# Performance work log

Measured on AMD Instinct MI355X. Metric: run time of the kernel, lower is better.

The kernel has to match this reference:

```python
import jax, jax.numpy as jnp
import numpy as np

EPS = 1e-6
B, H, S, D = 8, 16, 4096, 64


def setup_inputs() -> dict:
    key = jax.random.key(0)
    k1, k2, k3 = jax.random.split(key, 3)
    return {
        "keys": jax.random.normal(k1, (B, H, S, D), dtype=jnp.float32),
        "values": jax.random.normal(k2, (B, H, S, D), dtype=jnp.float32),
        "queries": jax.random.normal(k3, (B, H, S, D), dtype=jnp.float32),
    }


def reference(keys, values, queries):
    # update: accumulate outer-product associative memory per (batch, head)
    # M[b,h] = sum_s k_s outer v_s  -> [B, H, D, D]
    M = jnp.einsum("bhsd,bhse->bhde", keys, values)
    # normalizer z[b,h] = sum_s k_s -> [B, H, D]
    z = jnp.sum(keys, axis=2)
    # retrieve: out = (q @ M) / (q . z + eps)
    num = jnp.einsum("bhqd,bhde->bhqe", queries, M)        # [B, H, S, D]
    den = jnp.einsum("bhqd,bhd->bhq", queries, z) + EPS     # [B, H, S]
    return num / den[..., None]
```

## Files before the change

### kernel.cpp

```cpp
#include <hip/hip_runtime.h>

constexpr int Bc = 8, Hc = 16, Sc = 4096, Dc = 64;
constexpr int BH = Bc * Hc;
constexpr int STG = 16;
constexpr int MM = Dc * Dc;
constexpr int QT = 128;

template<int SSL>
__global__ __launch_bounds__(256, 4) void k1_accum(const float* __restrict__ K,
                                                   const float* __restrict__ V,
                                                   float* __restrict__ Pm,
                                                   double* __restrict__ Pz) {
  constexpr int CH = Sc / SSL;
  constexpr int NS = CH / STG;
  const int blk = blockIdx.x;
  const int bh = blk / SSL;
  const int ck = blk % SSL;
  const size_t base = ((size_t)bh * Sc + (size_t)ck * CH) * Dc;
  const float4* gk4 = (const float4*)(K + base);
  const float4* gv4 = (const float4*)(V + base);

  __shared__ __align__(16) float smem[4096];

  const int tid = threadIdx.x;
  const int w = tid >> 6;
  const int l = tid & 63;
  const int d0 = (l >> 3) * 8;
  const int e0 = (l & 7) * 8;

  float acc[8][8] = {};
  double zacc = 0.0;

  const int srow = tid >> 4;
  const int scol = (tid & 15) * 4;

  float4 rk = gk4[tid], rv = gv4[tid];
  *(float4*)&smem[srow * 64 + scol] = rk;
  *(float4*)&smem[2048 + srow * 64 + scol] = rv;
  __syncthreads();

  for (int st = 0; st < NS; ++st) {
    const int cur = st & 1, nxt = cur ^ 1;
    if (st + 1 < NS) {
      rk = gk4[(st + 1) * 256 + tid];
      rv = gv4[(st + 1) * 256 + tid];
    }
    const float* lkc = &smem[cur * 1024];
    const float* lvc = &smem[2048 + cur * 1024];
    #pragma unroll
    for (int r = 0; r < 4; ++r) {
      const int row = w * 4 + r;
      const float4 ka = *(const float4*)&lkc[row * 64 + d0];
      const float4 kb = *(const float4*)&lkc[row * 64 + d0 + 4];
      const float4 va = *(const float4*)&lvc[row * 64 + e0];
      const float4 vb = *(const float4*)&lvc[row * 64 + e0 + 4];
      const float kk[8] = {ka.x, ka.y, ka.z, ka.w, kb.x, kb.y, kb.z, kb.w};
      const float vv[8] = {va.x, va.y, va.z, va.w, vb.x, vb.y, vb.z, vb.w};
      #pragma unroll
      for (int a = 0; a < 8; ++a)
        #pragma unroll
        for (int b = 0; b < 8; ++b)
          acc[a][b] = fmaf(kk[a], vv[b], acc[a][b]);
    }
    #pragma unroll
    for (int r = 0; r < 4; ++r)
      zacc += (double)lkc[(w * 4 + r) * 64 + l];
    if (st + 1 < NS) {
      *(float4*)&smem[nxt * 1024 + srow * 64 + scol] = rk;
      *(float4*)&smem[2048 + nxt * 1024 + srow * 64 + scol] = rv;
    }
    __syncthreads();
  }

  #pragma unroll
  for (int p = 0; p < 4; ++p) {
    if (w == p) {
      #pragma unroll
      for (int a = 0; a < 8; ++a) {
        float* dst = &smem[(d0 + a) * 64 + e0];
        float4 lo = make_float4(acc[a][0], acc[a][1], acc[a][2], acc[a][3]);
        float4 hi = make_float4(acc[a][4], acc[a][5], acc[a][6], acc[a][7]);
        if (p == 0) {
          *(float4*)dst = lo; *(float4*)(dst + 4) = hi;
        } else {
          float4 olo = *(float4*)dst, ohi = *(float4*)(dst + 4);
          olo.x += lo.x; olo.y += lo.y; olo.z += lo.z; olo.w += lo.w;
          ohi.x += hi.x; ohi.y += hi.y; ohi.z += hi.z; ohi.w += hi.w;
          *(float4*)dst = olo; *(float4*)(dst + 4) = ohi;
        }
      }
    }
    __syncthreads();
  }

  float* pd = Pm + ((size_t)ck * BH + bh) * MM;
  #pragma unroll
  for (int j = 0; j < 4; ++j) {
    const int idx = tid + j * 256;
    ((float4*)pd)[idx] = *(const float4*)&smem[idx * 4];
  }
  Pz[((size_t)(ck * 4 + w) * BH + bh) * Dc + l] = zacc;
}

__global__ __launch_bounds__(256) void k2_reduce(const float* __restrict__ Pm,
                                                 const double* __restrict__ Pz,
                                                 float* __restrict__ Fm,
                                                 float* __restrict__ Fz,
                                                 int ss) {
  const int i = blockIdx.x * 256 + threadIdx.x;
  const int nm = BH * MM;
  if (i < nm) {
    float s = 0.f;
    for (int c = 0; c < ss; ++c) s += Pm[(size_t)c * nm + i];
    Fm[i] = s;
  }
  const int nz = BH * Dc;
  if (i < nz) {
    double s = 0.0;
    const int np = ss * 4;
    for (int c = 0; c < np; ++c) s += Pz[(size_t)c * nz + i];
    Fz[i] = (float)s;
  }
}

__global__ __launch_bounds__(256) void k3_retrieve(const float* __restrict__ Q,
                                                   const float* __restrict__ Fm,
                                                   const float* __restrict__ Fz,
                                                   float* __restrict__ O) {
  const int blk = blockIdx.x;
  const int bh = blk >> 5;
  const int row0 = (blk & 31) * QT;

  __shared__ __align__(16) float lm[Dc][Dc];
  __shared__ __align__(16) float lq[QT][68];
  __shared__ __align__(16) float lz[Dc];

  const int tid = threadIdx.x;

  const float4* gm4 = (const float4*)(Fm + (size_t)bh * MM);
  float4* lm4 = (float4*)&lm[0][0];
  #pragma unroll
  for (int j = 0; j < 4; ++j) lm4[tid + j * 256] = gm4[tid + j * 256];
  if (tid < Dc) lz[tid] = Fz[(size_t)bh * Dc + tid];

  const float4* gq4 = (const float4*)(Q + ((size_t)bh * Sc + row0) * Dc);
  #pragma unroll
  for (int j = 0; j < 8; ++j) {
    const int i4 = tid + j * 256;
    const float4 v = gq4[i4];
    const int f = i4 * 4;
    *(float4*)&lq[f >> 6][f & 63] = v;
  }
  __syncthreads();

  const int rg = tid >> 3;
  const int cg = tid & 7;
  const int r0 = rg * 4;
  const int e0 = cg * 8;

  float acc[4][8] = {};
  double den[4] = {0.0, 0.0, 0.0, 0.0};

  #pragma unroll
  for (int ds = 0; ds < 16; ++ds) {
    const int d0 = ds * 4;
    const float4 z4 = *(const float4*)&lz[d0];
    const float* zf = (const float*)&z4;
    float4 q4[4];
    #pragma unroll
    for (int r = 0; r < 4; ++r) q4[r] = *(const float4*)&lq[r0 + r][d0];
    const float* qf[4] = {(const float*)&q4[0], (const float*)&q4[1],
                          (const float*)&q4[2], (const float*)&q4[3]};
    #pragma unroll
    for (int i = 0; i < 4; ++i) {
      const float4 ma = *(const float4*)&lm[d0 + i][e0];
      const float4 mb = *(const float4*)&lm[d0 + i][e0 + 4];
      const float mf[8] = {ma.x, ma.y, ma.z, ma.w, mb.x, mb.y, mb.z, mb.w};
      const double zd = (double)zf[i];
      #pragma unroll
      for (int r = 0; r < 4; ++r) {
        const float qs = qf[r][i];
        den[r] += (double)qs * zd;
        #pragma unroll
        for (int j = 0; j < 8; ++j)
          acc[r][j] = fmaf(qs, mf[j], acc[r][j]);
      }
    }
  }

  #pragma unroll
  for (int r = 0; r < 4; ++r) {
    const double iv = 1.0 / (den[r] + 1e-6);
    float* go = O + ((size_t)bh * Sc + row0 + r0 + r) * Dc + e0;
    ((float4*)go)[0] = make_float4((float)((double)acc[r][0] * iv),
                                   (float)((double)acc[r][1] * iv),
                                   (float)((double)acc[r][2] * iv),
                                   (float)((double)acc[r][3] * iv));
    ((float4*)go)[1] = make_float4((float)((double)acc[r][4] * iv),
                                   (float)((double)acc[r][5] * iv),
                                   (float)((double)acc[r][6] * iv),
                                   (float)((double)acc[r][7] * iv));
  }
}

extern "C" void kernel_launch(void* const* d_in, const int* in_sizes, int n_in,
                              void* d_out, int out_size, void* d_ws, size_t ws_size,
                              hipStream_t stream) {
  const float* K = (const float*)d_in[0];
  const float* V = (const float*)d_in[1];
  const float* Q = (const float*)d_in[2];
  float* O = (float*)d_out;

  const size_t need16 = (size_t)16 * BH * MM * 4 + (size_t)BH * MM * 4 +
                        (size_t)16 * 4 * BH * Dc * 8 + (size_t)BH * Dc * 4;
  const int ss = (ws_size >= need16) ? 16 : 8;

  float* Pm = (float*)d_ws;
  float* Fm = Pm + (size_t)ss * BH * MM;
  double* Pz = (double*)(Fm + (size_t)BH * MM);
  float* Fz = (float*)(Pz + (size_t)ss * 4 * BH * Dc);

  if (ss == 16)
    hipLaunchKernelGGL(k1_accum<16>, dim3(BH * 16), dim3(256), 0, stream, K, V, Pm, Pz);
  else
    hipLaunchKernelGGL(k1_accum<8>, dim3(BH * 8), dim3(256), 0, stream, K, V, Pm, Pz);
  hipLaunchKernelGGL(k2_reduce, dim3((BH * MM + 255) / 256), dim3(256), 0, stream, Pm, Pz, Fm, Fz, ss);
  hipLaunchKernelGGL(k3_retrieve, dim3(BH * (Sc / QT)), dim3(256), 0, stream, Q, Fm, Fz, O);
}
```

Baseline: 192.5 us.

## Load K/V rows directly per wave with register double-buffering, drop LDS staging

The accumulation kernel no longer stages K/V tiles through shared memory with block-wide barriers. Each wave now streams its own contiguous range of rows straight from global memory into registers, using a two-deep software pipeline of loads. The split count is fixed at 8 chunks instead of choosing 16 from workspace size, and the reduction loops are unrolled with compile-time trip counts. This removes LDS traffic and per-stage syncs, but each lane issues many redundant global loads (64 lanes read the same row), depends on cache for reuse, and has half the blocks to hide latency.

```diff
diff --git a/kernel.cpp b/kernel.cpp
--- a/kernel.cpp
+++ b/kernel.cpp
@@ -2,76 +2,71 @@
 
 constexpr int Bc = 8, Hc = 16, Sc = 4096, Dc = 64;
 constexpr int BH = Bc * Hc;
-constexpr int STG = 16;
+constexpr int SS = 8;
+constexpr int CHUNK = Sc / SS;
+constexpr int WROWS = CHUNK / 4;
 constexpr int MM = Dc * Dc;
+constexpr int NZP = SS * 4;
 constexpr int QT = 128;
 
-template<int SSL>
-__global__ __launch_bounds__(256, 4) void k1_accum(const float* __restrict__ K,
-                                                   const float* __restrict__ V,
-                                                   float* __restrict__ Pm,
-                                                   double* __restrict__ Pz) {
-  constexpr int CH = Sc / SSL;
-  constexpr int NS = CH / STG;
+__global__ __launch_bounds__(256) void k1_accum(const float* __restrict__ K,
+                                                const float* __restrict__ V,
+                                                float* __restrict__ Pm,
+                                                double* __restrict__ Pz) {
   const int blk = blockIdx.x;
-  const int bh = blk / SSL;
-  const int ck = blk % SSL;
-  const size_t base = ((size_t)bh * Sc + (size_t)ck * CH) * Dc;
-  const float4* gk4 = (const float4*)(K + base);
-  const float4* gv4 = (const float4*)(V + base);
-
-  __shared__ __align__(16) float smem[4096];
-
+  const int bh = blk >> 3;
+  const int ck = blk & 7;
   const int tid = threadIdx.x;
   const int w = tid >> 6;
   const int l = tid & 63;
   const int d0 = (l >> 3) * 8;
   const int e0 = (l & 7) * 8;
 
+  const size_t rbase = ((size_t)bh * Sc + (size_t)ck * CHUNK + (size_t)w * WROWS) * Dc;
+  const float* kp = K + rbase;
+  const float* vp = V + rbase;
+
   float acc[8][8] = {};
   double zacc = 0.0;
 
-  const int srow = tid >> 4;
-  const int scol = (tid & 15) * 4;
-
-  float4 rk = gk4[tid], rv = gv4[tid];
-  *(float4*)&smem[srow * 64 + scol] = rk;
-  *(float4*)&smem[2048 + srow * 64 + scol] = rv;
-  __syncthreads();
-
-  for (int st = 0; st < NS; ++st) {
-    const int cur = st & 1, nxt = cur ^ 1;
-    if (st + 1 < NS) {
-      rk = gk4[(st + 1) * 256 + tid];
-      rv = gv4[(st + 1) * 256 + tid];
-    }
-    const float* lkc = &smem[cur * 1024];
-    const float* lvc = &smem[2048 + cur * 1024];
-    #pragma unroll
-    for (int r = 0; r < 4; ++r) {
-      const int row = w * 4 + r;
-      const float4 ka = *(const float4*)&lkc[row * 64 + d0];
-      const float4 kb = *(const float4*)&lkc[row * 64 + d0 + 4];
-      const float4 va = *(const float4*)&lvc[row * 64 + e0];
-      const float4 vb = *(const float4*)&lvc[row * 64 + e0 + 4];
-      const float kk[8] = {ka.x, ka.y, ka.z, ka.w, kb.x, kb.y, kb.z, kb.w};
-      const float vv[8] = {va.x, va.y, va.z, va.w, vb.x, vb.y, vb.z, vb.w};
-      #pragma unroll
-      for (int a = 0; a < 8; ++a)
-        #pragma unroll
-        for (int b = 0; b < 8; ++b)
-          acc[a][b] = fmaf(kk[a], vv[b], acc[a][b]);
-    }
-    #pragma unroll
-    for (int r = 0; r < 4; ++r)
-      zacc += (double)lkc[(w * 4 + r) * 64 + l];
-    if (st + 1 < NS) {
-      *(float4*)&smem[nxt * 1024 + srow * 64 + scol] = rk;
-      *(float4*)&smem[2048 + nxt * 1024 + srow * 64 + scol] = rv;
-    }
-    __syncthreads();
-  }
-
+  float4 ka0, kb0, va0, vb0; float z0;
+  float4 ka1, kb1, va1, vb1; float z1;
+
+#define K1_LOAD(S, r)                                                  \
+  ka##S = *(const float4*)(kp + (size_t)(r) * 64 + d0);                \
+  kb##S = *(const float4*)(kp + (size_t)(r) * 64 + d0 + 4);            \
+  va##S = *(const float4*)(vp + (size_t)(r) * 64 + e0);                \
+  vb##S = *(const float4*)(vp + (size_t)(r) * 64 + e0 + 4);            \
+  z##S = kp[(size_t)(r) * 64 + l];
+
+#define K1_COMP(S)                                                     \
+  {                                                                    \
+    const float kk[8] = {ka##S.x, ka##S.y, ka##S.z, ka##S.w,           \
+                         kb##S.x, kb##S.y, kb##S.z, kb##S.w};          \
+    const float vv[8] = {va##S.x, va##S.y, va##S.z, va##S.w,           \
+                         vb##S.x, vb##S.y, vb##S.z, vb##S.w};          \
+    _Pragma("unroll")                                                  \
+    for (int a = 0; a < 8; ++a)                                        \
+      _Pragma("unroll")                                                \
+      for (int b = 0; b < 8; ++b)                                      \
+        acc[a][b] = fmaf(kk[a], vv[b], acc[a][b]);                     \
+    zacc += (double)z##S;                                              \
+  }
+
+  K1_LOAD(0, 0)
+  K1_LOAD(1, 1)
+  for (int r = 0; r < WROWS - 2; r += 2) {
+    K1_COMP(0)
+    K1_LOAD(0, r + 2)
+    K1_COMP(1)
+    K1_LOAD(1, r + 3)
+  }
+  K1_COMP(0)
+  K1_COMP(1)
+#undef K1_LOAD
+#undef K1_COMP
+
+  __shared__ __align__(16) float smem[MM];
   #pragma unroll
   for (int p = 0; p < 4; ++p) {
     if (w == p) {
@@ -105,20 +100,20 @@
 __global__ __launch_bounds__(256) void k2_reduce(const float* __restrict__ Pm,
                                                  const double* __restrict__ Pz,
                                                  float* __restrict__ Fm,
-                                                 float* __restrict__ Fz,
-                                                 int ss) {
+                                                 float* __restrict__ Fz) {
   const int i = blockIdx.x * 256 + threadIdx.x;
   const int nm = BH * MM;
   if (i < nm) {
     float s = 0.f;
-    for (int c = 0; c < ss; ++c) s += Pm[(size_t)c * nm + i];
+    #pragma unroll
+    for (int c = 0; c < SS; ++c) s += Pm[(size_t)c * nm + i];
     Fm[i] = s;
   }
   const int nz = BH * Dc;
   if (i < nz) {
     double s = 0.0;
-    const int np = ss * 4;
-    for (int c = 0; c < np; ++c) s += Pz[(size_t)c * nz + i];
+    #pragma unroll
+    for (int c = 0; c < NZP; ++c) s += Pz[(size_t)c * nz + i];
     Fz[i] = (float)s;
   }
 }
@@ -211,19 +206,12 @@
   const float* Q = (const float*)d_in[2];
   float* O = (float*)d_out;
 
-  const size_t need16 = (size_t)16 * BH * MM * 4 + (size_t)BH * MM * 4 +
-                        (size_t)16 * 4 * BH * Dc * 8 + (size_t)BH * Dc * 4;
-  const int ss = (ws_size >= need16) ? 16 : 8;
-
   float* Pm = (float*)d_ws;
-  float* Fm = Pm + (size_t)ss * BH * MM;
+  float* Fm = Pm + (size_t)SS * BH * MM;
   double* Pz = (double*)(Fm + (size_t)BH * MM);
-  float* Fz = (float*)(Pz + (size_t)ss * 4 * BH * Dc);
-
-  if (ss == 16)
-    hipLaunchKernelGGL(k1_accum<16>, dim3(BH * 16), dim3(256), 0, stream, K, V, Pm, Pz);
-  else
-    hipLaunchKernelGGL(k1_accum<8>, dim3(BH * 8), dim3(256), 0, stream, K, V, Pm, Pz);
-  hipLaunchKernelGGL(k2_reduce, dim3((BH * MM + 255) / 256), dim3(256), 0, stream, Pm, Pz, Fm, Fz, ss);
+  float* Fz = (float*)(Pz + (size_t)NZP * BH * Dc);
+
+  hipLaunchKernelGGL(k1_accum, dim3(BH * SS), dim3(256), 0, stream, K, V, Pm, Pz);
+  hipLaunchKernelGGL(k2_reduce, dim3((BH * MM + 255) / 256), dim3(256), 0, stream, Pm, Pz, Fm, Fz);
   hipLaunchKernelGGL(k3_retrieve, dim3(BH * (Sc / QT)), dim3(256), 0, stream, Q, Fm, Fz, O);
 }
```

Result: slower. 222.5 us (+15.6%).
